# Performance work log

Hardware: AMD Instinct MI355X
Metric: run time of the kernel (lower is better)

The kernel has to match this reference:

```python
import jax, jax.numpy as jnp
import numpy as np

B, S, C = 2, 4096, 640
HEADS = 10
DH = C // HEADS  # 64
SCALE = 1.0 / np.sqrt(DH).astype(np.float32)


def setup_inputs() -> dict:
    key = jax.random.key(0)
    ks = jax.random.split(key, 5)
    w_std = 0.02
    return {
        "hidden_states": jax.random.normal(ks[0], (B, S, C), dtype=jnp.float32),
        "Wq": jax.random.normal(ks[1], (C, C), dtype=jnp.float32) * w_std,
        "Wk": jax.random.normal(ks[2], (C, C), dtype=jnp.float32) * w_std,
        "Wv": jax.random.normal(ks[3], (C, C), dtype=jnp.float32) * w_std,
        "Wo": jax.random.normal(ks[4], (C, C), dtype=jnp.float32) * w_std,
        "b_out": jnp.zeros((C,), dtype=jnp.float32),
    }


def _split_heads(x):
    # [B, S, C] -> [B, H, S, Dh]
    b, s, c = x.shape
    return x.reshape(b, s, HEADS, DH).transpose(0, 2, 1, 3)


def reference(hidden_states, Wq, Wk, Wv, Wo, b_out):
    residual = hidden_states
    # Linear projections (torch nn.Linear: x @ W.T), to_q/k/v have no bias
    q = jnp.einsum("bsc,dc->bsd", hidden_states, Wq)
    k = jnp.einsum("bsc,dc->bsd", hidden_states, Wk)
    v = jnp.einsum("bsc,dc->bsd", hidden_states, Wv)
    q = _split_heads(q)  # [B, H, S, Dh]
    k = _split_heads(k)
    v = _split_heads(v)
    # get_attention_scores: scaled QK^T + softmax (full O(S^2) matrix)
    scores = jnp.einsum("bhqd,bhkd->bhqk", q, k) * SCALE
    probs = jax.nn.softmax(scores, axis=-1)
    out = jnp.einsum("bhqk,bhkd->bhqd", probs, v)  # [B, H, S, Dh]
    # batch_to_head_dim: [B, H, S, Dh] -> [B, S, C]
    out = out.transpose(0, 2, 1, 3).reshape(hidden_states.shape)
    # to_out[0] Linear (with bias), to_out[1] Dropout = identity at eval
    out = jnp.einsum("bsc,dc->bsd", out, Wo) + b_out
    # residual_connection=True, rescale_output_factor=1.0
    return out + residual
```

## Files before the change

kernel.cpp:

```cpp
#include <hip/hip_runtime.h>
#include <stdint.h>
#include <stddef.h>

#define Bsz 2
#define Ssz 4096
#define Csz 640
#define Hn 10
#define Dh 64
#define NSPLIT 4
#define QROWS 81920

typedef __attribute__((ext_vector_type(8))) short bf16x8;
typedef __attribute__((ext_vector_type(4))) float f32x4;
typedef __attribute__((ext_vector_type(16))) float f32x16;
typedef __attribute__((ext_vector_type(2))) unsigned int u32x2;

typedef __attribute__((address_space(1))) void as1_void;
typedef __attribute__((address_space(3))) void as3_void;

__device__ __forceinline__ void async16(const void* g, void* l) {
  __builtin_amdgcn_global_load_lds((as1_void*)(g), (as3_void*)(l), 16, 0, 0);
}

__device__ __forceinline__ ushort f2bf(float f) {
  union { float f; uint32_t u; } v; v.f = f;
  return (ushort)((v.u + 0x7FFFu + ((v.u >> 16) & 1u)) >> 16);
}

__device__ __forceinline__ uint32_t pack_bf16(float lo, float hi) {
  return __builtin_amdgcn_perm(__float_as_uint(hi), __float_as_uint(lo), 0x07060302u);
}

__device__ __forceinline__ float bf_lo(uint32_t u) {
  return __uint_as_float(u << 16);
}
__device__ __forceinline__ float bf_hi(uint32_t u) {
  return __uint_as_float(u & 0xFFFF0000u);
}

__device__ __forceinline__ float fast_exp2(float x) {
#if __has_builtin(__builtin_amdgcn_exp2f)
  return __builtin_amdgcn_exp2f(x);
#else
  return __exp2f(x);
#endif
}

#define QSCALE 0.1803368801111204f

__global__ __launch_bounds__(256) void cvt_bf16(const float* __restrict__ in,
                                                ushort* __restrict__ out, int n4) {
  int i = blockIdx.x * 256 + threadIdx.x;
  if (i < n4) {
    const float4 v = ((const float4*)in)[i];
    ushort4 o;
    o.x = f2bf(v.x); o.y = f2bf(v.y); o.z = f2bf(v.z); o.w = f2bf(v.w);
    ((ushort4*)out)[i] = o;
  }
}

__global__ __launch_bounds__(256) void cvt4_bf16(
    const float* __restrict__ i0, const float* __restrict__ i1,
    const float* __restrict__ i2, const float* __restrict__ i3,
    ushort* __restrict__ o0, ushort* __restrict__ o1,
    ushort* __restrict__ o2, ushort* __restrict__ o3, int n4) {
  const float* in = (blockIdx.y == 0) ? i0 : (blockIdx.y == 1) ? i1
                    : (blockIdx.y == 2) ? i2 : i3;
  ushort* out = (blockIdx.y == 0) ? o0 : (blockIdx.y == 1) ? o1
                : (blockIdx.y == 2) ? o2 : o3;
  int i = blockIdx.x * 256 + threadIdx.x;
  if (i < n4) {
    const float4 v = ((const float4*)in)[i];
    ushort4 o;
    o.x = f2bf(v.x); o.y = f2bf(v.y); o.z = f2bf(v.z); o.w = f2bf(v.w);
    ((ushort4*)out)[i] = o;
  }
}

template<int MODE>
__global__ __launch_bounds__(256) void gemm_k(
    const ushort* __restrict__ A, const ushort* __restrict__ W0,
    const ushort* __restrict__ W1, const ushort* __restrict__ W2,
    ushort* __restrict__ Qh, ushort* __restrict__ Kh, ushort* __restrict__ Vt,
    const float* __restrict__ bias, const float* __restrict__ residual,
    float* __restrict__ outf)
{
  __shared__ ushort As[128 * 64];
  __shared__ ushort Bs[128 * 64];
  const int t = threadIdx.x;
  const int lane = t & 63;
  const int w = t >> 6;
  const int quad = lane >> 4;
  const int l15 = lane & 15;
  const int m0 = blockIdx.x * 128;
  const int wub = t & ~63;

  int n0, mat;
  const ushort* W;
  if (MODE == 0) {
    mat = blockIdx.y / 5;
    n0 = (blockIdx.y % 5) * 128;
    W = (mat == 0) ? W0 : ((mat == 1) ? W1 : W2);
  } else {
    mat = 0;
    n0 = blockIdx.y * 128;
    W = W0;
  }
  const int qm = (w >> 1) * 64;
  const int qn = (w & 1) * 64;

  f32x4 acc[4][4];
  const f32x4 zero4 = {0.f, 0.f, 0.f, 0.f};
#pragma unroll
  for (int i = 0; i < 4; ++i)
#pragma unroll
    for (int j = 0; j < 4; ++j) acc[i][j] = zero4;

  for (int k0 = 0; k0 < Csz; k0 += 64) {
    __syncthreads();
#pragma unroll
    for (int s = 0; s < 4; ++s) {
      int L = s * 256 + t;
      int row = L >> 3, pc = L & 7;
      int c = pc ^ (row & 7);
      async16(A + (size_t)(m0 + row) * Csz + k0 + c * 8,
              (char*)As + (s * 256 + wub) * 16);
    }
#pragma unroll
    for (int s = 0; s < 4; ++s) {
      int L = s * 256 + t;
      int row = L >> 3, pc = L & 7;
      int c = pc ^ (row & 7);
      async16(W + (size_t)(n0 + row) * Csz + k0 + c * 8,
              (char*)Bs + (s * 256 + wub) * 16);
    }
    __syncthreads();
#pragma unroll
    for (int ks = 0; ks < 2; ++ks) {
      bf16x8 af[4], bfr[4];
#pragma unroll
      for (int i = 0; i < 4; ++i) {
        int row = qm + i * 16 + l15;
        int pc = (ks * 4 + quad) ^ (row & 7);
        af[i] = *(const bf16x8*)(As + row * 64 + pc * 8);
      }
#pragma unroll
      for (int j = 0; j < 4; ++j) {
        int row = qn + j * 16 + l15;
        int pc = (ks * 4 + quad) ^ (row & 7);
        bfr[j] = *(const bf16x8*)(Bs + row * 64 + pc * 8);
      }
#pragma unroll
      for (int i = 0; i < 4; ++i)
#pragma unroll
        for (int j = 0; j < 4; ++j)
          acc[i][j] = __builtin_amdgcn_mfma_f32_16x16x32_bf16(af[i], bfr[j], acc[i][j], 0, 0, 0);
    }
  }

  if (MODE == 0) {
    if (mat < 2) {
      ushort* __restrict__ dst = (mat == 0) ? Qh : Kh;
      const float sc = (mat == 0) ? QSCALE : 1.0f;
#pragma unroll
      for (int j = 0; j < 4; ++j) {
        int n = n0 + qn + j * 16 + l15;
        int h = n >> 6, dh = n & 63;
#pragma unroll
        for (int i = 0; i < 4; ++i) {
#pragma unroll
          for (int r = 0; r < 4; ++r) {
            int m = m0 + qm + i * 16 + quad * 4 + r;
            int b = m >> 12, sidx = m & 4095;
            dst[(((size_t)b * Hn + h) * Ssz + sidx) * Dh + dh] = f2bf(acc[i][j][r] * sc);
          }
        }
      }
    } else {
#pragma unroll
      for (int j = 0; j < 4; ++j) {
        int n = n0 + qn + j * 16 + l15;
        int h = n >> 6, dh = n & 63;
#pragma unroll
        for (int i = 0; i < 4; ++i) {
          int mb = m0 + qm + i * 16 + quad * 4;
          int b = mb >> 12, sidx = mb & 4095;
          ushort4 pk;
          pk.x = f2bf(acc[i][j][0]); pk.y = f2bf(acc[i][j][1]);
          pk.z = f2bf(acc[i][j][2]); pk.w = f2bf(acc[i][j][3]);
          *(ushort4*)(Vt + (((size_t)b * Hn + h) * Dh + dh) * Ssz + sidx) = pk;
        }
      }
    }
  } else {
#pragma unroll
    for (int j = 0; j < 4; ++j) {
      int n = n0 + qn + j * 16 + l15;
      float bs = bias[n];
#pragma unroll
      for (int i = 0; i < 4; ++i) {
#pragma unroll
        for (int r = 0; r < 4; ++r) {
          int m = m0 + qm + i * 16 + quad * 4 + r;
          size_t idx = (size_t)m * Csz + n;
          outf[idx] = acc[i][j][r] + bs + residual[idx];
        }
      }
    }
  }
}

__global__ __launch_bounds__(256, 4) void attn_k(
    const ushort* __restrict__ Qh, const ushort* __restrict__ Kh,
    const ushort* __restrict__ Vt, ushort* __restrict__ Opart,
    float* __restrict__ lpart)
{
  __shared__ ushort Ks[2][64 * 64];
  __shared__ ushort Vs[2][64 * 64];

  const int t = threadIdx.x;
  const int lane = t & 63;
  const int w = t >> 6;
  const int l31 = lane & 31;
  const int hi = lane >> 5;

  const int g = blockIdx.x;
  const int jj = g >> 3;
  const int x = jj & 31;
  const int team = (g & 7) + ((jj >> 5) << 3);
  const int bh = team % 20;
  const int z = team / 20;

  const size_t qk_off = (size_t)bh * Ssz * Dh;
  const size_t v_off = (size_t)bh * Dh * Ssz;
  const int qbase = x * 128 + w * 32;
  const int kvbase = z * (Ssz / NSPLIT);

  bf16x8 qf[4];
  {
    int q = qbase + l31;
#pragma unroll
    for (int ks = 0; ks < 4; ++ks)
      qf[ks] = *(const bf16x8*)(Qh + qk_off + (size_t)q * Dh + ks * 16 + hi * 8);
  }

  f32x16 z16;
#pragma unroll
  for (int i = 0; i < 16; ++i) z16[i] = 0.f;

  f32x16 Oa[2];
  Oa[0] = z16; Oa[1] = z16;
  float lpx = 0.f, lpy = 0.f;

  int ka[4];
#pragma unroll
  for (int ks = 0; ks < 4; ++ks)
    ka[ks] = l31 * 128 + (((ks * 2 + hi) ^ (l31 & 7)) << 4);

  const int row8 = lane >> 3;
  const int pcs = lane & 7;
#define STAGE(bi, kv)                                                          \
  {                                                                            \
    _Pragma("unroll") for (int s = 0; s < 2; ++s) {                            \
      int i = w * 2 + s;                                                       \
      int row = i * 8 + row8;                                                  \
      int c = pcs ^ (row & 7);                                                 \
      async16(Kh + qk_off + (size_t)(kvbase + (kv) + row) * Dh + c * 8,        \
              (char*)&Ks[bi][0] + i * 1024);                                   \
    }                                                                          \
    _Pragma("unroll") for (int s = 0; s < 2; ++s) {                            \
      int i = w * 2 + s;                                                       \
      int row = i * 8 + row8;                                                  \
      int c = pcs ^ (row & 7);                                                 \
      async16(Vt + v_off + (size_t)row * Ssz + kvbase + (kv) + c * 8,          \
              (char*)&Vs[bi][0] + i * 1024);                                   \
    }                                                                          \
  }

  STAGE(0, 0);

  const char* Kbase = (const char*)&Ks[0][0];
  const char* Vbase = (const char*)&Vs[0][0];

  const int NIT = (Ssz / NSPLIT) / 64;
  for (int it = 0; it < NIT; ++it) {
    const int cb = it & 1;
    asm volatile("s_barrier" ::: "memory");
    if (it + 1 < NIT) {
      STAGE(cb ^ 1, (it + 1) * 64);
      asm volatile("s_waitcnt vmcnt(4)" ::: "memory");
    } else {
      asm volatile("s_waitcnt vmcnt(0)" ::: "memory");
    }
    asm volatile("s_barrier" ::: "memory");

    const int cbo = cb * 8192;

#pragma unroll
    for (int tau = 0; tau < 2; ++tau) {
      f32x16 Sq;
#pragma unroll
      for (int ks = 0; ks < 4; ++ks) {
        bf16x8 kf = *(const bf16x8*)(Kbase + cbo + tau * 4096 + ka[ks]);
        Sq = __builtin_amdgcn_mfma_f32_32x32x16_bf16(kf, qf[ks],
                                                     ks == 0 ? z16 : Sq, 0, 0, 0);
      }
      uint32_t pk[8];
#pragma unroll
      for (int a = 0; a < 8; ++a) {
        float p0 = fast_exp2(Sq[2 * a]);
        float p1 = fast_exp2(Sq[2 * a + 1]);
        lpx += p0; lpy += p1;
        pk[a] = pack_bf16(p0, p1);
      }

#pragma unroll
      for (int k2 = 0; k2 < 2; ++k2) {
        const int ks2 = tau * 2 + k2;
        const int bA = (2 * ks2) & 3;
        const int bB = (2 * ks2 + 1) & 3;
        u32x2 r0 = __builtin_amdgcn_permlane32_swap(pk[2 * bA],
                                                    pk[2 * bB], false, false);
        u32x2 r1 = __builtin_amdgcn_permlane32_swap(pk[2 * bA + 1],
                                                    pk[2 * bB + 1], false, false);
        union { uint32_t u[4]; bf16x8 v; } pu;
        pu.u[0] = r0.x; pu.u[1] = r1.x;
        pu.u[2] = r0.y; pu.u[3] = r1.y;
        bf16x8 pf = pu.v;
#pragma unroll
        for (int mt = 0; mt < 2; ++mt) {
          bf16x8 vfr = *(const bf16x8*)(Vbase + cbo + mt * 4096 + ka[ks2]);
          Oa[mt] = __builtin_amdgcn_mfma_f32_32x32x16_bf16(vfr, pf, Oa[mt], 0, 0, 0);
        }
      }
    }
  }
#undef STAGE

  const size_t prow_base = (size_t)z * QROWS + (size_t)bh * Ssz;
  float l_part = lpx + lpy;
  float l_tot = l_part + __shfl_xor(l_part, 32, 64);
  int q = qbase + l31;
  if (hi == 0) lpart[prow_base + q] = l_tot;
  ushort* dst = Opart + (prow_base + q) * 64;
#pragma unroll
  for (int mt = 0; mt < 2; ++mt) {
#pragma unroll
    for (int gg = 0; gg < 4; ++gg) {
      int dh0 = mt * 32 + 8 * gg + 4 * hi;
      uint2 val;
      val.x = pack_bf16(Oa[mt][4 * gg + 0], Oa[mt][4 * gg + 1]);
      val.y = pack_bf16(Oa[mt][4 * gg + 2], Oa[mt][4 * gg + 3]);
      *(uint2*)(dst + dh0) = val;
    }
  }
}

__global__ __launch_bounds__(256) void combine_k(
    const ushort* __restrict__ Opart, const float* __restrict__ lpart,
    ushort* __restrict__ attnb)
{
  int gid = blockIdx.x * 256 + threadIdx.x;
  int row = gid >> 4;
  int dh0 = (gid & 15) * 4;
  int bh = row >> 12, q = row & 4095;
  int b = bh / Hn, h = bh % Hn;
  float a0 = 0.f, a1 = 0.f, a2 = 0.f, a3 = 0.f, lsum = 0.f;
#pragma unroll
  for (int sp = 0; sp < NSPLIT; ++sp) {
    uint2 v = *(const uint2*)(Opart + ((size_t)sp * QROWS + row) * 64 + dh0);
    a0 += bf_lo(v.x); a1 += bf_hi(v.x);
    a2 += bf_lo(v.y); a3 += bf_hi(v.y);
    lsum += lpart[(size_t)sp * QROWS + row];
  }
  float inv = 1.0f / lsum;
  uint2 o;
  o.x = pack_bf16(a0 * inv, a1 * inv);
  o.y = pack_bf16(a2 * inv, a3 * inv);
  *(uint2*)(attnb + ((size_t)b * Ssz + q) * Csz + h * Dh + dh0) = o;
}

extern "C" void kernel_launch(void* const* d_in, const int* in_sizes, int n_in,
                              void* d_out, int out_size, void* d_ws, size_t ws_size,
                              hipStream_t stream) {
  (void)in_sizes; (void)n_in; (void)out_size; (void)ws_size;
  const float* hs = (const float*)d_in[0];
  const float* Wq = (const float*)d_in[1];
  const float* Wk = (const float*)d_in[2];
  const float* Wv = (const float*)d_in[3];
  const float* Wo = (const float*)d_in[4];
  const float* bo = (const float*)d_in[5];
  float* out = (float*)d_out;

  char* ws = (char*)d_ws;
  ushort* Xbf = (ushort*)(ws);
  ushort* Wqb = (ushort*)(ws + 10485760);
  ushort* Wkb = (ushort*)(ws + 10485760 + 819200);
  ushort* Wvb = (ushort*)(ws + 10485760 + 2 * 819200);
  ushort* Wob = (ushort*)(ws + 10485760 + 3 * 819200);
  ushort* Qh  = (ushort*)(ws + 13762560);
  ushort* Kh  = (ushort*)(ws + 13762560 + 10485760);
  ushort* Vt  = (ushort*)(ws + 13762560 + 2 * 10485760);
  ushort* attnb = (ushort*)(ws + 13762560 + 3 * 10485760);
  ushort* Opart = (ushort*)(ws + 55705600);
  float*  lpart = (float*)(ws + 55705600 + 41943040);

  hipLaunchKernelGGL(cvt_bf16, dim3(5120), dim3(256), 0, stream, hs, Xbf, 1310720);
  hipLaunchKernelGGL(cvt4_bf16, dim3(400, 4), dim3(256), 0, stream,
                     Wq, Wk, Wv, Wo, Wqb, Wkb, Wvb, Wob, 102400);

  hipLaunchKernelGGL((gemm_k<0>), dim3(64, 15), dim3(256), 0, stream,
                     Xbf, Wqb, Wkb, Wvb, Qh, Kh, Vt, (const float*)nullptr,
                     (const float*)nullptr, (float*)nullptr);
  hipLaunchKernelGGL(attn_k, dim3(2560), dim3(256), 0, stream,
                     Qh, Kh, Vt, Opart, lpart);
  hipLaunchKernelGGL(combine_k, dim3(QROWS / 16), dim3(256), 0, stream,
                     Opart, lpart, attnb);
  hipLaunchKernelGGL((gemm_k<1>), dim3(64, 5), dim3(256), 0, stream,
                     attnb, Wob, (const ushort*)nullptr, (const ushort*)nullptr,
                     (ushort*)nullptr, (ushort*)nullptr, (ushort*)nullptr,
                     bo, hs, out);
}
```

Measured before the change: 241.1 us.

## Compute softmax row sums via MFMA with ones, merge conversion kernels, unroll KV loop by two

The per-lane scalar accumulation of exponentiated scores is replaced by an extra MFMA that multiplies a ones vector by the packed bf16 probabilities. This moves the row-sum work onto the matrix unit and removes the cross-lane shuffle at the end. The two fp32-to-bf16 conversion kernels are merged into one launch, and the attention KV loop is unrolled by two so buffer offsets become compile-time constants. The trade-off is one more MFMA per P tile and row sums taken over bf16-rounded probabilities rather than fp32 values.

After: 236.8 us. No clear change (-1.8%).

```diff
diff --git a/kernel.cpp b/kernel.cpp
--- a/kernel.cpp
+++ b/kernel.cpp
@@ -48,33 +48,32 @@
 
 #define QSCALE 0.1803368801111204f
 
-__global__ __launch_bounds__(256) void cvt_bf16(const float* __restrict__ in,
-                                                ushort* __restrict__ out, int n4) {
-  int i = blockIdx.x * 256 + threadIdx.x;
-  if (i < n4) {
-    const float4 v = ((const float4*)in)[i];
-    ushort4 o;
-    o.x = f2bf(v.x); o.y = f2bf(v.y); o.z = f2bf(v.z); o.w = f2bf(v.w);
-    ((ushort4*)out)[i] = o;
-  }
-}
-
-__global__ __launch_bounds__(256) void cvt4_bf16(
-    const float* __restrict__ i0, const float* __restrict__ i1,
-    const float* __restrict__ i2, const float* __restrict__ i3,
-    ushort* __restrict__ o0, ushort* __restrict__ o1,
-    ushort* __restrict__ o2, ushort* __restrict__ o3, int n4) {
-  const float* in = (blockIdx.y == 0) ? i0 : (blockIdx.y == 1) ? i1
-                    : (blockIdx.y == 2) ? i2 : i3;
-  ushort* out = (blockIdx.y == 0) ? o0 : (blockIdx.y == 1) ? o1
-                : (blockIdx.y == 2) ? o2 : o3;
-  int i = blockIdx.x * 256 + threadIdx.x;
-  if (i < n4) {
-    const float4 v = ((const float4*)in)[i];
-    ushort4 o;
-    o.x = f2bf(v.x); o.y = f2bf(v.y); o.z = f2bf(v.z); o.w = f2bf(v.w);
-    ((ushort4*)out)[i] = o;
-  }
+__global__ __launch_bounds__(256) void cvt_all(
+    const float* __restrict__ hs, const float* __restrict__ Wq,
+    const float* __restrict__ Wk, const float* __restrict__ Wv,
+    const float* __restrict__ Wo, ushort* __restrict__ Xbf,
+    ushort* __restrict__ Wqb, ushort* __restrict__ Wkb,
+    ushort* __restrict__ Wvb, ushort* __restrict__ Wob)
+{
+  int gb = blockIdx.x;
+  const float* in;
+  ushort* out;
+  int i;
+  if (gb < 5120) {
+    in = hs; out = Xbf;
+    i = gb * 256 + threadIdx.x;
+  } else {
+    int wj = gb - 5120;
+    int mat = wj / 400;
+    int rb = wj - mat * 400;
+    in  = (mat == 0) ? Wq  : (mat == 1) ? Wk  : (mat == 2) ? Wv  : Wo;
+    out = (mat == 0) ? Wqb : (mat == 1) ? Wkb : (mat == 2) ? Wvb : Wob;
+    i = rb * 256 + threadIdx.x;
+  }
+  const float4 v = ((const float4*)in)[i];
+  ushort4 o;
+  o.x = f2bf(v.x); o.y = f2bf(v.y); o.z = f2bf(v.z); o.w = f2bf(v.w);
+  ((ushort4*)out)[i] = o;
 }
 
 template<int MODE>
@@ -250,7 +249,11 @@
 
   f32x16 Oa[2];
   Oa[0] = z16; Oa[1] = z16;
-  float lpx = 0.f, lpy = 0.f;
+  f32x16 La = z16;
+
+  bf16x8 onesf;
+#pragma unroll
+  for (int i = 0; i < 8; ++i) onesf[i] = (short)0x3F80;
 
   int ka[4];
 #pragma unroll
@@ -282,66 +285,68 @@
   const char* Kbase = (const char*)&Ks[0][0];
   const char* Vbase = (const char*)&Vs[0][0];
 
-  const int NIT = (Ssz / NSPLIT) / 64;
-  for (int it = 0; it < NIT; ++it) {
-    const int cb = it & 1;
-    asm volatile("s_barrier" ::: "memory");
-    if (it + 1 < NIT) {
-      STAGE(cb ^ 1, (it + 1) * 64);
-      asm volatile("s_waitcnt vmcnt(4)" ::: "memory");
-    } else {
-      asm volatile("s_waitcnt vmcnt(0)" ::: "memory");
-    }
-    asm volatile("s_barrier" ::: "memory");
-
-    const int cbo = cb * 8192;
-
-#pragma unroll
-    for (int tau = 0; tau < 2; ++tau) {
-      f32x16 Sq;
-#pragma unroll
-      for (int ks = 0; ks < 4; ++ks) {
-        bf16x8 kf = *(const bf16x8*)(Kbase + cbo + tau * 4096 + ka[ks]);
-        Sq = __builtin_amdgcn_mfma_f32_32x32x16_bf16(kf, qf[ks],
-                                                     ks == 0 ? z16 : Sq, 0, 0, 0);
-      }
-      uint32_t pk[8];
-#pragma unroll
-      for (int a = 0; a < 8; ++a) {
-        float p0 = fast_exp2(Sq[2 * a]);
-        float p1 = fast_exp2(Sq[2 * a + 1]);
-        lpx += p0; lpy += p1;
-        pk[a] = pack_bf16(p0, p1);
-      }
-
-#pragma unroll
-      for (int k2 = 0; k2 < 2; ++k2) {
-        const int ks2 = tau * 2 + k2;
-        const int bA = (2 * ks2) & 3;
-        const int bB = (2 * ks2 + 1) & 3;
-        u32x2 r0 = __builtin_amdgcn_permlane32_swap(pk[2 * bA],
-                                                    pk[2 * bB], false, false);
-        u32x2 r1 = __builtin_amdgcn_permlane32_swap(pk[2 * bA + 1],
-                                                    pk[2 * bB + 1], false, false);
-        union { uint32_t u[4]; bf16x8 v; } pu;
-        pu.u[0] = r0.x; pu.u[1] = r1.x;
-        pu.u[2] = r0.y; pu.u[3] = r1.y;
-        bf16x8 pf = pu.v;
-#pragma unroll
-        for (int mt = 0; mt < 2; ++mt) {
-          bf16x8 vfr = *(const bf16x8*)(Vbase + cbo + mt * 4096 + ka[ks2]);
-          Oa[mt] = __builtin_amdgcn_mfma_f32_32x32x16_bf16(vfr, pf, Oa[mt], 0, 0, 0);
-        }
-      }
-    }
-  }
+#define ITER(IT, CB, CBO, DO_STAGE)                                            \
+  {                                                                            \
+    asm volatile("s_barrier" ::: "memory");                                    \
+    if (DO_STAGE) {                                                            \
+      STAGE((CB) ^ 1, ((IT) + 1) * 64);                                        \
+      asm volatile("s_waitcnt vmcnt(4)" ::: "memory");                         \
+    } else {                                                                   \
+      asm volatile("s_waitcnt vmcnt(0)" ::: "memory");                         \
+    }                                                                          \
+    asm volatile("s_barrier" ::: "memory");                                    \
+    _Pragma("unroll")                                                          \
+    for (int tau = 0; tau < 2; ++tau) {                                        \
+      f32x16 Sq;                                                               \
+      _Pragma("unroll")                                                        \
+      for (int ks = 0; ks < 4; ++ks) {                                         \
+        bf16x8 kf = *(const bf16x8*)(Kbase + (CBO) + tau * 4096 + ka[ks]);     \
+        Sq = __builtin_amdgcn_mfma_f32_32x32x16_bf16(                          \
+            kf, qf[ks], ks == 0 ? z16 : Sq, 0, 0, 0);                          \
+      }                                                                        \
+      uint32_t pk[8];                                                          \
+      _Pragma("unroll")                                                        \
+      for (int a = 0; a < 8; ++a) {                                            \
+        float p0 = fast_exp2(Sq[2 * a]);                                       \
+        float p1 = fast_exp2(Sq[2 * a + 1]);                                   \
+        pk[a] = pack_bf16(p0, p1);                                             \
+      }                                                                        \
+      _Pragma("unroll")                                                        \
+      for (int k2 = 0; k2 < 2; ++k2) {                                         \
+        const int ks2 = tau * 2 + k2;                                          \
+        const int bA = (2 * ks2) & 3;                                          \
+        const int bB = (2 * ks2 + 1) & 3;                                      \
+        u32x2 r0 = __builtin_amdgcn_permlane32_swap(pk[2 * bA],                \
+                                                    pk[2 * bB], false, false); \
+        u32x2 r1 = __builtin_amdgcn_permlane32_swap(pk[2 * bA + 1],            \
+                                                    pk[2 * bB + 1], false, false); \
+        union { uint32_t u[4]; bf16x8 v; } pu;                                 \
+        pu.u[0] = r0.x; pu.u[1] = r1.x;                                        \
+        pu.u[2] = r0.y; pu.u[3] = r1.y;                                        \
+        bf16x8 pf = pu.v;                                                      \
+        La = __builtin_amdgcn_mfma_f32_32x32x16_bf16(onesf, pf, La, 0, 0, 0);  \
+        _Pragma("unroll")                                                      \
+        for (int mt = 0; mt < 2; ++mt) {                                       \
+          bf16x8 vfr = *(const bf16x8*)(Vbase + (CBO) + mt * 4096 + ka[ks2]);  \
+          Oa[mt] = __builtin_amdgcn_mfma_f32_32x32x16_bf16(vfr, pf, Oa[mt],    \
+                                                           0, 0, 0);           \
+        }                                                                      \
+      }                                                                        \
+    }                                                                          \
+  }
+
+  const int NH = (Ssz / NSPLIT) / 128;
+  for (int itp = 0; itp < NH; ++itp) {
+    const int it0 = itp * 2;
+    ITER(it0, 0, 0, 1);
+    ITER(it0 + 1, 1, 8192, (itp + 1 < NH));
+  }
+#undef ITER
 #undef STAGE
 
   const size_t prow_base = (size_t)z * QROWS + (size_t)bh * Ssz;
-  float l_part = lpx + lpy;
-  float l_tot = l_part + __shfl_xor(l_part, 32, 64);
   int q = qbase + l31;
-  if (hi == 0) lpart[prow_base + q] = l_tot;
+  if (hi == 0) lpart[prow_base + q] = La[0];
   ushort* dst = Opart + (prow_base + q) * 64;
 #pragma unroll
   for (int mt = 0; mt < 2; ++mt) {
@@ -405,9 +410,8 @@
   ushort* Opart = (ushort*)(ws + 55705600);
   float*  lpart = (float*)(ws + 55705600 + 41943040);
 
-  hipLaunchKernelGGL(cvt_bf16, dim3(5120), dim3(256), 0, stream, hs, Xbf, 1310720);
-  hipLaunchKernelGGL(cvt4_bf16, dim3(400, 4), dim3(256), 0, stream,
-                     Wq, Wk, Wv, Wo, Wqb, Wkb, Wvb, Wob, 102400);
+  hipLaunchKernelGGL(cvt_all, dim3(6720), dim3(256), 0, stream,
+                     hs, Wq, Wk, Wv, Wo, Xbf, Wqb, Wkb, Wvb, Wob);
 
   hipLaunchKernelGGL((gemm_k<0>), dim3(64, 15), dim3(256), 0, stream,
                      Xbf, Wqb, Wkb, Wvb, Qh, Kh, Vt, (const float*)nullptr,
```
